# Performance work log

Hardware: AMD Instinct MI355X
Metric: run time of the kernel (lower is better)

The kernel has to match this reference:

```python
import jax, jax.numpy as jnp
import numpy as np

B, N, C = 128, 2048, 3
VL, PN = 256, 128  # vector_length, prediction_num
NEG_SLOPE = 0.01   # torch LeakyReLU default
BN_EPS = 1e-5


def _lin(key, fin, fout):
    k1, k2 = jax.random.split(key)
    lim = 1.0 / np.sqrt(fin)
    W = jax.random.uniform(k1, (fin, fout), minval=-lim, maxval=lim, dtype=jnp.float32)
    b = jax.random.uniform(k2, (fout,), minval=-lim, maxval=lim, dtype=jnp.float32)
    return W, b


def setup_inputs() -> dict:
    key = jax.random.key(0)
    ks = jax.random.split(key, 14)
    x = jax.random.normal(ks[0], (B, N, C), dtype=jnp.float32)
    lengths = jnp.maximum(jax.random.randint(ks[1], (B,), 0, N), 1).astype(jnp.int32)
    eps = jax.random.normal(ks[2], (B, VL), dtype=jnp.float32)
    W1, b1 = _lin(ks[3], C, 64)
    W2, b2 = _lin(ks[4], 64, 64)
    W3, b3 = _lin(ks[5], 64, 128)
    W4, b4 = _lin(ks[6], 128, 1024)
    Wf, bf = _lin(ks[7], 1024, 1024)
    Wmu, bmu = _lin(ks[8], 1024, VL)
    Wlv, blv = _lin(ks[9], 1024, VL)
    Wd1, bd1 = _lin(ks[10], VL, 1024)
    Wd2, bd2 = _lin(ks[11], 1024, 1024)
    Wd3, bd3 = _lin(ks[12], 1024, PN * C)
    g1 = jnp.ones((1024,), jnp.float32); be1 = jnp.zeros((1024,), jnp.float32)
    g2 = jnp.ones((1024,), jnp.float32); be2 = jnp.zeros((1024,), jnp.float32)
    return dict(x=x, lengths=lengths, eps=eps,
                W1=W1, b1=b1, W2=W2, b2=b2, W3=W3, b3=b3, W4=W4, b4=b4,
                Wf=Wf, bf=bf, Wmu=Wmu, bmu=bmu, Wlv=Wlv, blv=blv,
                Wd1=Wd1, bd1=bd1, g1=g1, be1=be1,
                Wd2=Wd2, bd2=bd2, g2=g2, be2=be2,
                Wd3=Wd3, bd3=bd3)


def _lrelu(h):
    return jnp.where(h > 0, h, NEG_SLOPE * h)


def _bn(h, g, b):
    # BatchNorm1d in training mode: biased batch stats
    m = h.mean(axis=0)
    v = h.var(axis=0)
    return (h - m) * jax.lax.rsqrt(v + BN_EPS) * g + b


def reference(x, lengths, eps,
              W1, b1, W2, b2, W3, b3, W4, b4,
              Wf, bf, Wmu, bmu, Wlv, blv,
              Wd1, bd1, g1, be1, Wd2, bd2, g2, be2, Wd3, bd3):
    # --- pointnet per-point MLP (batched over padded [B,N,C]) ---
    h = _lrelu(x @ W1 + b1)          # [B,N,64]
    h = _lrelu(h @ W2 + b2)          # [B,N,64]
    h = _lrelu(h @ W3 + b3)          # [B,N,128]
    h = _lrelu(h @ W4 + b4)          # [B,N,1024]
    # masked max over points (ragged -> padded+mask)
    mask = jnp.arange(N)[None, :] < lengths[:, None]   # [B,N]
    h = jnp.where(mask[:, :, None], h, -jnp.inf)
    pooled = jnp.max(h, axis=1)      # [B,1024]
    # --- encoder head ---
    e = _lrelu(pooled @ Wf + bf)
    mu = e @ Wmu + bmu               # [B,VL]
    logvar = e @ Wlv + blv           # [B,VL]
    # --- reparameterize ---
    z = mu + eps * jnp.exp(0.5 * logvar)
    # --- decoder: Linear+BN+LeakyReLU x2, final Linear ---
    d = _lrelu(_bn(z @ Wd1 + bd1, g1, be1))
    d = _lrelu(_bn(d @ Wd2 + bd2, g2, be2))
    y = (d @ Wd3 + bd3).reshape(-1, PN, C)   # [B,PN,C]
    return (y, mu, logvar)
```

## Files before the change

### kernel.cpp

```cpp
#include <hip/hip_runtime.h>
#include <hip/hip_bf16.h>
#include <math.h>

#define NEG_SLOPE 0.01f

typedef short short8 __attribute__((ext_vector_type(8)));
typedef float f32x4 __attribute__((ext_vector_type(4)));

__device__ __forceinline__ float lrelu(float v) { return v > 0.0f ? v : NEG_SLOPE * v; }

__device__ __forceinline__ short f2bf(float f) {
    __hip_bfloat16 h = __float2bfloat16(f);
    return __builtin_bit_cast(short, h);
}

__global__ __launch_bounds__(256) void pack_all(
    const float* __restrict__ W4, const float* __restrict__ Wf,
    const float* __restrict__ Wmu, const float* __restrict__ Wlv,
    const float* __restrict__ Wd1, const float* __restrict__ Wd2,
    const float* __restrict__ Wd3, const float* __restrict__ W2,
    const float* __restrict__ W3,
    short* __restrict__ F4, short* __restrict__ Ff, short* __restrict__ Fmuvl,
    short* __restrict__ Fd1, short* __restrict__ Fd2, short* __restrict__ Fd3,
    short* __restrict__ F2, short* __restrict__ F3)
{
    int bid = blockIdx.x;
    const float* src = nullptr; short* dst = nullptr; int K = 0, N = 0; int muvl = 0;
    if      (bid < 64)   { src = W4;  dst = F4;    K = 128;  N = 1024; }
    else if (bid < 576)  { src = Wf;  dst = Ff;    K = 1024; N = 1024; bid -= 64; }
    else if (bid < 832)  { src = nullptr; dst = Fmuvl; K = 1024; N = 512; muvl = 1; bid -= 576; }
    else if (bid < 960)  { src = Wd1; dst = Fd1;   K = 256;  N = 1024; bid -= 832; }
    else if (bid < 1472) { src = Wd2; dst = Fd2;   K = 1024; N = 1024; bid -= 960; }
    else if (bid < 1664) { src = Wd3; dst = Fd3;   K = 1024; N = 384;  bid -= 1472; }
    else if (bid < 1666) { src = W2;  dst = F2;    K = 64;   N = 64;   bid -= 1664; }
    else                 { src = W3;  dst = F3;    K = 64;   N = 128;  bid -= 1666; }

    const int fragid = bid * 4 + (threadIdx.x >> 6);
    const int lane   = threadIdx.x & 63;
    const int K32    = K >> 5;
    const int t   = fragid / (K32 * 4);
    const int rem = fragid - t * K32 * 4;
    const int ks  = rem >> 2;
    const int n   = rem & 3;
    const int col   = t * 64 + n * 16 + (lane & 15);
    const int kbase = ks * 32 + (lane >> 4) * 8;

    short8 v;
#pragma unroll
    for (int e = 0; e < 8; ++e) {
        float f;
        if (muvl) f = (col < 256) ? Wmu[(size_t)(kbase + e) * 256 + col]
                                  : Wlv[(size_t)(kbase + e) * 256 + col - 256];
        else      f = src[(size_t)(kbase + e) * N + col];
        v[e] = f2bf(f);
    }
    *(short8*)&dst[(size_t)fragid * 512 + lane * 8] = v;
}

__global__ __launch_bounds__(128, 2) void h3_kernel(
    const float* __restrict__ x, const int* __restrict__ lengths,
    const float* __restrict__ W1, const float* __restrict__ b1,
    const float* __restrict__ b2, const float* __restrict__ b3,
    const short* __restrict__ F2, const short* __restrict__ F3,
    short* __restrict__ h3p)
{
    const int tid  = threadIdx.x;
    const int b    = blockIdx.x & 127;
    const int c2   = blockIdx.x >> 7;
    const int lane = tid & 63;
    const int w    = tid >> 6;
    const int g    = c2 * 2 + w;
    const int len  = lengths[b];
    if (g * 64 >= len) return;

    __shared__ short S[16384];
    short* Aw = S + w * 8192;
    const int gid = b * 2048 + g * 64 + lane;

    {
        const float x0 = x[gid * 3 + 0];
        const float x1 = x[gid * 3 + 1];
        const float x2 = x[gid * 3 + 2];
#pragma unroll
        for (int q = 0; q < 8; ++q) {
            short8 pv;
#pragma unroll
            for (int e = 0; e < 8; ++e) {
                int c = q * 8 + e;
                float v = b1[c];
                v = fmaf(x0, W1[c], v);
                v = fmaf(x1, W1[64 + c], v);
                v = fmaf(x2, W1[128 + c], v);
                pv[e] = f2bf(lrelu(v));
            }
            *(short8*)&Aw[lane * 64 + ((q ^ (lane & 7)) * 8)] = pv;
        }
    }

    {
        short8 a2[4][2];
#pragma unroll
        for (int m = 0; m < 4; ++m)
#pragma unroll
            for (int ks = 0; ks < 2; ++ks) {
                int rl = m * 16 + (lane & 15);
                int kch = ks * 4 + (lane >> 4);
                a2[m][ks] = *(const short8*)&Aw[rl * 64 + ((kch ^ (rl & 7)) * 8)];
            }
        short8 b2f[2][4];
#pragma unroll
        for (int ks = 0; ks < 2; ++ks)
#pragma unroll
            for (int n = 0; n < 4; ++n)
                b2f[ks][n] = *(const short8*)&F2[(size_t)(ks * 4 + n) * 512 + lane * 8];

        f32x4 acc2[4][4];
#pragma unroll
        for (int m = 0; m < 4; ++m)
#pragma unroll
            for (int n = 0; n < 4; ++n) acc2[m][n] = 0;
#pragma unroll
        for (int ks = 0; ks < 2; ++ks)
#pragma unroll
            for (int n = 0; n < 4; ++n)
#pragma unroll
                for (int m = 0; m < 4; ++m)
                    acc2[m][n] = __builtin_amdgcn_mfma_f32_16x16x32_bf16(
                        a2[m][ks], b2f[ks][n], acc2[m][n], 0, 0, 0);

#pragma unroll
        for (int n = 0; n < 4; ++n) {
            int col = n * 16 + (lane & 15);
            float bv = b2[col];
            int colch = col >> 3;
#pragma unroll
            for (int m = 0; m < 4; ++m)
#pragma unroll
                for (int r = 0; r < 4; ++r) {
                    int rl = m * 16 + (lane >> 4) * 4 + r;
                    Aw[4096 + rl * 64 + ((colch ^ (rl & 7)) * 8) + (col & 7)] =
                        f2bf(lrelu(acc2[m][n][r] + bv));
                }
        }
    }

    {
        short8 a3[4][2];
#pragma unroll
        for (int m = 0; m < 4; ++m)
#pragma unroll
            for (int ks = 0; ks < 2; ++ks) {
                int rl = m * 16 + (lane & 15);
                int kch = ks * 4 + (lane >> 4);
                a3[m][ks] = *(const short8*)&Aw[4096 + rl * 64 + ((kch ^ (rl & 7)) * 8)];
            }
#pragma unroll
        for (int half = 0; half < 2; ++half) {
            short8 b3f[2][4];
#pragma unroll
            for (int ks = 0; ks < 2; ++ks)
#pragma unroll
                for (int n = 0; n < 4; ++n)
                    b3f[ks][n] = *(const short8*)&F3[(size_t)(half * 8 + ks * 4 + n) * 512 + lane * 8];

            f32x4 acc3[4][4];
#pragma unroll
            for (int m = 0; m < 4; ++m)
#pragma unroll
                for (int n = 0; n < 4; ++n) acc3[m][n] = 0;
#pragma unroll
            for (int ks = 0; ks < 2; ++ks)
#pragma unroll
                for (int n = 0; n < 4; ++n)
#pragma unroll
                    for (int m = 0; m < 4; ++m)
                        acc3[m][n] = __builtin_amdgcn_mfma_f32_16x16x32_bf16(
                            a3[m][ks], b3f[ks][n], acc3[m][n], 0, 0, 0);

#pragma unroll
            for (int n = 0; n < 4; ++n) {
                int col = half * 64 + n * 16 + (lane & 15);
                float bv = b3[col];
                int colch = col >> 3;
#pragma unroll
                for (int m = 0; m < 4; ++m)
#pragma unroll
                    for (int r = 0; r < 4; ++r) {
                        int rl = m * 16 + (lane >> 4) * 4 + r;
                        Aw[rl * 128 + ((colch ^ (rl & 7)) * 8) + (col & 7)] =
                            f2bf(lrelu(acc3[m][n][r] + bv));
                    }
            }
        }
    }

    const size_t obase = ((size_t)(b * 32 + g) * 16) * 512 + lane * 8;
#pragma unroll
    for (int ks = 0; ks < 4; ++ks)
#pragma unroll
        for (int m = 0; m < 4; ++m) {
            int rl = m * 16 + (lane & 15);
            int ch = (ks * 4 + (lane >> 4)) ^ (rl & 7);
            short8 af = *(const short8*)&Aw[rl * 128 + ch * 8];
            *(short8*)&h3p[obase + (size_t)(ks * 4 + m) * 512] = af;
        }
}

__global__ __launch_bounds__(256, 3) void l4_pool_kernel(
    const short* __restrict__ h3p, const int* __restrict__ lengths,
    const short* __restrict__ F4, float* __restrict__ part)
{
    const int tid = threadIdx.x, lane = tid & 63, w = tid >> 6;
    const int b = blockIdx.x, ch = blockIdx.y, rh = blockIdx.z;
    const int len = lengths[b];
    const int live32 = (len + 31) >> 5;
    const int cbeg = rh * 32;
    int cend = (rh + 1) * 32; if (cend > live32) cend = live32;
    if (cbeg >= cend) return;

    __shared__ short L[8192];

    const int t = ch * 4 + w;
    short8 bfr[4][4];
#pragma unroll
    for (int ks = 0; ks < 4; ++ks)
#pragma unroll
        for (int n = 0; n < 4; ++n)
            bfr[ks][n] = *(const short8*)&F4[(size_t)((t * 4 + ks) * 4 + n) * 512 + lane * 8];

    const int cfull = len >> 5;
    float madd[2][4];
#pragma unroll
    for (int m = 0; m < 2; ++m)
#pragma unroll
        for (int rr = 0; rr < 4; ++rr)
            madd[m][rr] = (m * 16 + (lane >> 4) * 4 + rr < (len & 31)) ? 0.0f : -INFINITY;

    f32x4 rmax[4];
#pragma unroll
    for (int n = 0; n < 4; ++n)
#pragma unroll
        for (int rr = 0; rr < 4; ++rr) rmax[n][rr] = -INFINITY;

    const size_t bb = (size_t)b * 32;
    short8 stg[2];
    {
        int c64 = cbeg >> 1, mh = cbeg & 1;
#pragma unroll
        for (int pass = 0; pass < 2; ++pass) {
            int idx = pass * 256 + tid, fi = idx >> 6, li = idx & 63;
            stg[pass] = *(const short8*)&h3p[((bb + c64) * 16 + (fi >> 1) * 4 + mh * 2 + (fi & 1)) * 512 + li * 8];
        }
#pragma unroll
        for (int pass = 0; pass < 2; ++pass)
            *(short8*)&L[(pass * 256 + tid) * 8] = stg[pass];
    }
    __syncthreads();

    for (int c = cbeg; c < cend; ++c) {
        const int p = (c - cbeg) & 1;
        if (c + 1 < cend) {
            int c64 = (c + 1) >> 1, mh = (c + 1) & 1;
#pragma unroll
            for (int pass = 0; pass < 2; ++pass) {
                int idx = pass * 256 + tid, fi = idx >> 6, li = idx & 63;
                stg[pass] = *(const short8*)&h3p[((bb + c64) * 16 + (fi >> 1) * 4 + mh * 2 + (fi & 1)) * 512 + li * 8];
            }
        }

        const short* Lb = L + p * 4096;
        f32x4 acc[2][4];
#pragma unroll
        for (int m = 0; m < 2; ++m)
#pragma unroll
            for (int n = 0; n < 4; ++n) acc[m][n] = 0;
#pragma unroll
        for (int ks = 0; ks < 4; ++ks) {
            short8 a0 = *(const short8*)&Lb[(ks * 2 + 0) * 512 + lane * 8];
            short8 a1 = *(const short8*)&Lb[(ks * 2 + 1) * 512 + lane * 8];
#pragma unroll
            for (int n = 0; n < 4; ++n) {
                acc[0][n] = __builtin_amdgcn_mfma_f32_16x16x32_bf16(a0, bfr[ks][n], acc[0][n], 0, 0, 0);
                acc[1][n] = __builtin_amdgcn_mfma_f32_16x16x32_bf16(a1, bfr[ks][n], acc[1][n], 0, 0, 0);
            }
        }
        if (c < cfull) {
#pragma unroll
            for (int n = 0; n < 4; ++n)
#pragma unroll
                for (int rr = 0; rr < 4; ++rr)
                    rmax[n][rr] = fmaxf(rmax[n][rr], fmaxf(acc[0][n][rr], acc[1][n][rr]));
        } else {
#pragma unroll
            for (int n = 0; n < 4; ++n)
#pragma unroll
                for (int rr = 0; rr < 4; ++rr)
                    rmax[n][rr] = fmaxf(rmax[n][rr],
                        fmaxf(acc[0][n][rr] + madd[0][rr], acc[1][n][rr] + madd[1][rr]));
        }
        __syncthreads();
        if (c + 1 < cend) {
            short* Ln = L + (p ^ 1) * 4096;
#pragma unroll
            for (int pass = 0; pass < 2; ++pass)
                *(short8*)&Ln[(pass * 256 + tid) * 8] = stg[pass];
            __syncthreads();
        }
    }

#pragma unroll
    for (int n = 0; n < 4; ++n) {
        float v = fmaxf(fmaxf(rmax[n][0], rmax[n][1]), fmaxf(rmax[n][2], rmax[n][3]));
        v = fmaxf(v, __shfl_xor(v, 16));
        v = fmaxf(v, __shfl_xor(v, 32));
        if (lane < 16)
            part[((size_t)b * 2 + rh) * 1024 + ch * 256 + w * 64 + n * 16 + lane] = v;
    }
}

__global__ __launch_bounds__(256) void reduce_pool_kernel(
    const float* __restrict__ part, const int* __restrict__ lengths,
    const float* __restrict__ b4, short* __restrict__ pooled)
{
    const int b = blockIdx.x;
    const bool two = lengths[b] > 1024;
    for (int i = threadIdx.x; i < 1024; i += 256) {
        float m = part[((size_t)b * 2 + 0) * 1024 + i];
        if (two) m = fmaxf(m, part[((size_t)b * 2 + 1) * 1024 + i]);
        pooled[(size_t)b * 1024 + i] = f2bf(lrelu(m + b4[i]));
    }
}

template<int K32, int EPI>
__global__ __launch_bounds__(64) void gemm16(
    const short* __restrict__ A, const short* __restrict__ Wfrag,
    const float* __restrict__ bias, const float* __restrict__ bias2,
    float* __restrict__ outF, float* __restrict__ outF2,
    short* __restrict__ outB, int Nout)
{
    const int lane = threadIdx.x;
    const int cbb = blockIdx.x, rh = blockIdx.y;
    const int K = K32 * 32;
    const int t = cbb >> 2, n = cbb & 3;

    short8 bf[K32];
#pragma unroll
    for (int ks = 0; ks < K32; ++ks)
        bf[ks] = *(const short8*)&Wfrag[(size_t)((t * K32 + ks) * 4 + n) * 512 + lane * 8];

    const int arow0 = rh * 32 + (lane & 15);
    const int koff  = (lane >> 4) * 8;
    f32x4 acc[2];
    acc[0] = 0; acc[1] = 0;
#pragma unroll
    for (int ks = 0; ks < K32; ++ks) {
        short8 a0 = *(const short8*)&A[(size_t)arow0 * K + ks * 32 + koff];
        short8 a1 = *(const short8*)&A[(size_t)(arow0 + 16) * K + ks * 32 + koff];
        acc[0] = __builtin_amdgcn_mfma_f32_16x16x32_bf16(a0, bf[ks], acc[0], 0, 0, 0);
        acc[1] = __builtin_amdgcn_mfma_f32_16x16x32_bf16(a1, bf[ks], acc[1], 0, 0, 0);
    }

    const int c0 = cbb * 16;
    const int cl = lane & 15;
    if (EPI == 2) {
        const float* bs = (c0 < 256) ? bias : bias2;
        float* of = (c0 < 256) ? outF : outF2;
        int col = (c0 & 255) + cl;
        float bv = bs[col];
#pragma unroll
        for (int m = 0; m < 2; ++m)
#pragma unroll
            for (int rr = 0; rr < 4; ++rr) {
                int row = rh * 32 + m * 16 + (lane >> 4) * 4 + rr;
                of[(size_t)row * 256 + col] = acc[m][rr] + bv;
            }
    } else {
        int col = c0 + cl;
        float bv = bias[col];
#pragma unroll
        for (int m = 0; m < 2; ++m)
#pragma unroll
            for (int rr = 0; rr < 4; ++rr) {
                int row = rh * 32 + m * 16 + (lane >> 4) * 4 + rr;
                float v = acc[m][rr] + bv;
                if (EPI == 1) outB[(size_t)row * Nout + col] = f2bf(lrelu(v));
                else          outF[(size_t)row * Nout + col] = v;
            }
    }
}

template<int K32, bool ZIN>
__global__ __launch_bounds__(256) void gemmBN(
    const short* __restrict__ A, const float* __restrict__ muv,
    const float* __restrict__ lvv, const float* __restrict__ eps,
    const short* __restrict__ Wfrag,
    const float* __restrict__ g, const float* __restrict__ be,
    short* __restrict__ outB, int Nout)
{
    __shared__ float bns[4][16];
    __shared__ float bnq[4][16];

    const int tid = threadIdx.x, lane = tid & 63, w = tid >> 6;
    const int cbb = blockIdx.x;
    const int K = K32 * 32;
    const int t = cbb >> 2, n = cbb & 3;

    short8 bf[K32];
#pragma unroll
    for (int ks = 0; ks < K32; ++ks)
        bf[ks] = *(const short8*)&Wfrag[(size_t)((t * K32 + ks) * 4 + n) * 512 + lane * 8];

    const int arow0 = w * 32 + (lane & 15);
    const int koff  = (lane >> 4) * 8;
    f32x4 acc[2];
    acc[0] = 0; acc[1] = 0;
#pragma unroll
    for (int ks = 0; ks < K32; ++ks) {
        short8 a0, a1;
        if (ZIN) {
#pragma unroll
            for (int e = 0; e < 8; ++e) {
                int k = ks * 32 + koff + e;
                size_t i0 = (size_t)arow0 * 256 + k;
                size_t i1 = (size_t)(arow0 + 16) * 256 + k;
                a0[e] = f2bf(fmaf(eps[i0], expf(0.5f * lvv[i0]), muv[i0]));
                a1[e] = f2bf(fmaf(eps[i1], expf(0.5f * lvv[i1]), muv[i1]));
            }
        } else {
            a0 = *(const short8*)&A[(size_t)arow0 * K + ks * 32 + koff];
            a1 = *(const short8*)&A[(size_t)(arow0 + 16) * K + ks * 32 + koff];
        }
        acc[0] = __builtin_amdgcn_mfma_f32_16x16x32_bf16(a0, bf[ks], acc[0], 0, 0, 0);
        acc[1] = __builtin_amdgcn_mfma_f32_16x16x32_bf16(a1, bf[ks], acc[1], 0, 0, 0);
    }

    float s = 0.f, q = 0.f;
#pragma unroll
    for (int m = 0; m < 2; ++m)
#pragma unroll
        for (int rr = 0; rr < 4; ++rr) {
            float v = acc[m][rr];
            s += v; q = fmaf(v, v, q);
        }
    s += __shfl_xor(s, 16); s += __shfl_xor(s, 32);
    q += __shfl_xor(q, 16); q += __shfl_xor(q, 32);
    if (lane < 16) { bns[w][lane] = s; bnq[w][lane] = q; }
    __syncthreads();

    const int cl = lane & 15;
    float st = bns[0][cl] + bns[1][cl] + bns[2][cl] + bns[3][cl];
    float qt = bnq[0][cl] + bnq[1][cl] + bnq[2][cl] + bnq[3][cl];
    float mean = st * (1.0f / 128.0f);
    float var  = qt * (1.0f / 128.0f) - mean * mean;
    float rs   = 1.0f / sqrtf(var + 1e-5f);
    const int col = cbb * 16 + cl;
    float gg = g[col] * rs;
    float bb = be[col] - mean * gg;

#pragma unroll
    for (int m = 0; m < 2; ++m)
#pragma unroll
        for (int rr = 0; rr < 4; ++rr) {
            int row = w * 32 + m * 16 + (lane >> 4) * 4 + rr;
            outB[(size_t)row * Nout + col] = f2bf(lrelu(fmaf(acc[m][rr], gg, bb)));
        }
}

extern "C" void kernel_launch(void* const* d_in, const int* in_sizes, int n_in,
                              void* d_out, int out_size, void* d_ws, size_t ws_size,
                              hipStream_t stream)
{
    const float* x       = (const float*)d_in[0];
    const int*   lengths = (const int*)  d_in[1];
    const float* eps     = (const float*)d_in[2];
    const float* W1  = (const float*)d_in[3];  const float* b1  = (const float*)d_in[4];
    const float* W2  = (const float*)d_in[5];  const float* b2  = (const float*)d_in[6];
    const float* W3  = (const float*)d_in[7];  const float* b3  = (const float*)d_in[8];
    const float* W4  = (const float*)d_in[9];  const float* b4  = (const float*)d_in[10];
    const float* Wf  = (const float*)d_in[11]; const float* bf  = (const float*)d_in[12];
    const float* Wmu = (const float*)d_in[13]; const float* bmu = (const float*)d_in[14];
    const float* Wlv = (const float*)d_in[15]; const float* blv = (const float*)d_in[16];
    const float* Wd1 = (const float*)d_in[17];
    const float* g1  = (const float*)d_in[19]; const float* be1 = (const float*)d_in[20];
    const float* Wd2 = (const float*)d_in[21];
    const float* g2  = (const float*)d_in[23]; const float* be2 = (const float*)d_in[24];
    const float* Wd3 = (const float*)d_in[25]; const float* bd3 = (const float*)d_in[26];

    float* out = (float*)d_out;
    float* y_out  = out;
    float* mu_out = out + 49152;
    float* lv_out = out + 81920;

    char* ws = (char*)d_ws;
    short* F4    = (short*)(ws + 0);
    short* Ff    = (short*)(ws + 262144);
    short* Fmuvl = (short*)(ws + 2359296);
    short* Fd1   = (short*)(ws + 3407872);
    short* Fd2   = (short*)(ws + 3932160);
    short* Fd3   = (short*)(ws + 6029312);
    short* F2    = (short*)(ws + 6815744);
    short* F3    = (short*)(ws + 6823936);
    short* h3p   = (short*)(ws + 6840320);
    float* part  = (float*)(ws + 73949184);
    short* pooled = (short*)(ws + 74997760);
    short* ebuf   = (short*)(ws + 75259904);
    short* d1v    = (short*)(ws + 75522048);
    short* d2v    = (short*)(ws + 75784192);

    pack_all<<<1670, 256, 0, stream>>>(W4, Wf, Wmu, Wlv, Wd1, Wd2, Wd3, W2, W3,
                                       F4, Ff, Fmuvl, Fd1, Fd2, Fd3, F2, F3);
    h3_kernel<<<2048, 128, 0, stream>>>(x, lengths, W1, b1, b2, b3, F2, F3, h3p);
    l4_pool_kernel<<<dim3(128, 4, 2), 256, 0, stream>>>(h3p, lengths, F4, part);
    reduce_pool_kernel<<<128, 256, 0, stream>>>(part, lengths, b4, pooled);
    gemm16<32, 1><<<dim3(64, 4), 64, 0, stream>>>(pooled, Ff, bf, nullptr,
                                                  nullptr, nullptr, ebuf, 1024);
    gemm16<32, 2><<<dim3(32, 4), 64, 0, stream>>>(ebuf, Fmuvl, bmu, blv,
                                                  mu_out, lv_out, nullptr, 256);
    gemmBN<8, true><<<64, 256, 0, stream>>>(nullptr, mu_out, lv_out, eps,
                                            Fd1, g1, be1, d1v, 1024);
    gemmBN<32, false><<<64, 256, 0, stream>>>(d1v, nullptr, nullptr, nullptr,
                                              Fd2, g2, be2, d2v, 1024);
    gemm16<32, 0><<<dim3(24, 4), 64, 0, stream>>>(d2v, Fd3, bd3, nullptr,
                                                  y_out, nullptr, nullptr, 384);
}
```

Baseline: 122.6 us.

## Drop LDS staging in layer-4 pool; per-wave 128-col tiles with register double-buffering

The layer-4 GEMM+maxpool kernel no longer stages activations through shared memory with barriers. Each wave now loads its 16-row A fragments straight from global into registers, double-buffered, and covers 128 output columns, so the B fragments held in registers double. Work is split into 16-row chunks over 4 row-quarters instead of 32-row chunks over 2 halves, which trims masked waste on ragged lengths, and the reduce kernel combines up to 4 partials. Smaller buffers are moved into the no-longer-needed h3p region. The cost is more registers, with occupancy lowered to 2 blocks, and each wave reads A from global/L2 itself.

```diff
diff --git a/kernel.cpp b/kernel.cpp
--- a/kernel.cpp
+++ b/kernel.cpp
@@ -206,115 +206,91 @@
         }
 }
 
-__global__ __launch_bounds__(256, 3) void l4_pool_kernel(
+#define L4_LD(BUF, C)                                                         \
+    do {                                                                      \
+        const int g_ = (C) >> 2, m_ = (C) & 3;                                \
+        const size_t fb_ = ((size_t)(b * 32 + g_) * 16 + m_) * 512 + lane * 8;\
+        _Pragma("unroll")                                                     \
+        for (int ks = 0; ks < 4; ++ks)                                        \
+            BUF[ks] = *(const short8*)&h3p[fb_ + (size_t)(ks * 4) * 512];     \
+    } while (0)
+
+#define L4_FOLD(BUF, C)                                                       \
+    do {                                                                      \
+        f32x4 acc[8];                                                         \
+        _Pragma("unroll")                                                     \
+        for (int n = 0; n < 8; ++n) acc[n] = 0;                               \
+        _Pragma("unroll")                                                     \
+        for (int ks = 0; ks < 4; ++ks)                                        \
+            _Pragma("unroll")                                                 \
+            for (int n = 0; n < 8; ++n)                                       \
+                acc[n] = __builtin_amdgcn_mfma_f32_16x16x32_bf16(             \
+                    BUF[ks], bfr[ks][n], acc[n], 0, 0, 0);                    \
+        if ((C) == partial) {                                                 \
+            _Pragma("unroll")                                                 \
+            for (int n = 0; n < 8; ++n)                                       \
+                _Pragma("unroll")                                             \
+                for (int rr = 0; rr < 4; ++rr)                                \
+                    rmax[n][rr] = fmaxf(rmax[n][rr], acc[n][rr] + madd[rr]);  \
+        } else {                                                              \
+            _Pragma("unroll")                                                 \
+            for (int n = 0; n < 8; ++n)                                       \
+                _Pragma("unroll")                                             \
+                for (int rr = 0; rr < 4; ++rr)                                \
+                    rmax[n][rr] = fmaxf(rmax[n][rr], acc[n][rr]);             \
+        }                                                                     \
+    } while (0)
+
+__global__ __launch_bounds__(256, 2) void l4_pool_kernel(
     const short* __restrict__ h3p, const int* __restrict__ lengths,
     const short* __restrict__ F4, float* __restrict__ part)
 {
     const int tid = threadIdx.x, lane = tid & 63, w = tid >> 6;
-    const int b = blockIdx.x, ch = blockIdx.y, rh = blockIdx.z;
+    const int b = blockIdx.x, cgh = blockIdx.y, rq = blockIdx.z;
+    const int cg = cgh * 4 + w;
     const int len = lengths[b];
-    const int live32 = (len + 31) >> 5;
-    const int cbeg = rh * 32;
-    int cend = (rh + 1) * 32; if (cend > live32) cend = live32;
+    const int CH16 = (len + 15) >> 4;
+    const int cbeg = rq * 32;
+    int cend = cbeg + 32; if (cend > CH16) cend = CH16;
     if (cbeg >= cend) return;
 
-    __shared__ short L[8192];
-
-    const int t = ch * 4 + w;
-    short8 bfr[4][4];
+    short8 bfr[4][8];
 #pragma unroll
     for (int ks = 0; ks < 4; ++ks)
 #pragma unroll
-        for (int n = 0; n < 4; ++n)
-            bfr[ks][n] = *(const short8*)&F4[(size_t)((t * 4 + ks) * 4 + n) * 512 + lane * 8];
-
-    const int cfull = len >> 5;
-    float madd[2][4];
-#pragma unroll
-    for (int m = 0; m < 2; ++m)
-#pragma unroll
-        for (int rr = 0; rr < 4; ++rr)
-            madd[m][rr] = (m * 16 + (lane >> 4) * 4 + rr < (len & 31)) ? 0.0f : -INFINITY;
-
-    f32x4 rmax[4];
-#pragma unroll
-    for (int n = 0; n < 4; ++n)
+        for (int n = 0; n < 8; ++n)
+            bfr[ks][n] = *(const short8*)&F4[
+                (size_t)(((cg * 2 + (n >> 2)) * 4 + ks) * 4 + (n & 3)) * 512 + lane * 8];
+
+    const int partial = (len & 15) ? (CH16 - 1) : -1;
+    float madd[4];
+#pragma unroll
+    for (int rr = 0; rr < 4; ++rr)
+        madd[rr] = ((CH16 - 1) * 16 + (lane >> 4) * 4 + rr < len) ? 0.0f : -INFINITY;
+
+    f32x4 rmax[8];
+#pragma unroll
+    for (int n = 0; n < 8; ++n)
 #pragma unroll
         for (int rr = 0; rr < 4; ++rr) rmax[n][rr] = -INFINITY;
 
-    const size_t bb = (size_t)b * 32;
-    short8 stg[2];
-    {
-        int c64 = cbeg >> 1, mh = cbeg & 1;
-#pragma unroll
-        for (int pass = 0; pass < 2; ++pass) {
-            int idx = pass * 256 + tid, fi = idx >> 6, li = idx & 63;
-            stg[pass] = *(const short8*)&h3p[((bb + c64) * 16 + (fi >> 1) * 4 + mh * 2 + (fi & 1)) * 512 + li * 8];
-        }
-#pragma unroll
-        for (int pass = 0; pass < 2; ++pass)
-            *(short8*)&L[(pass * 256 + tid) * 8] = stg[pass];
-    }
-    __syncthreads();
-
-    for (int c = cbeg; c < cend; ++c) {
-        const int p = (c - cbeg) & 1;
-        if (c + 1 < cend) {
-            int c64 = (c + 1) >> 1, mh = (c + 1) & 1;
-#pragma unroll
-            for (int pass = 0; pass < 2; ++pass) {
-                int idx = pass * 256 + tid, fi = idx >> 6, li = idx & 63;
-                stg[pass] = *(const short8*)&h3p[((bb + c64) * 16 + (fi >> 1) * 4 + mh * 2 + (fi & 1)) * 512 + li * 8];
-            }
-        }
-
-        const short* Lb = L + p * 4096;
-        f32x4 acc[2][4];
-#pragma unroll
-        for (int m = 0; m < 2; ++m)
-#pragma unroll
-            for (int n = 0; n < 4; ++n) acc[m][n] = 0;
-#pragma unroll
-        for (int ks = 0; ks < 4; ++ks) {
-            short8 a0 = *(const short8*)&Lb[(ks * 2 + 0) * 512 + lane * 8];
-            short8 a1 = *(const short8*)&Lb[(ks * 2 + 1) * 512 + lane * 8];
-#pragma unroll
-            for (int n = 0; n < 4; ++n) {
-                acc[0][n] = __builtin_amdgcn_mfma_f32_16x16x32_bf16(a0, bfr[ks][n], acc[0][n], 0, 0, 0);
-                acc[1][n] = __builtin_amdgcn_mfma_f32_16x16x32_bf16(a1, bfr[ks][n], acc[1][n], 0, 0, 0);
-            }
-        }
-        if (c < cfull) {
-#pragma unroll
-            for (int n = 0; n < 4; ++n)
-#pragma unroll
-                for (int rr = 0; rr < 4; ++rr)
-                    rmax[n][rr] = fmaxf(rmax[n][rr], fmaxf(acc[0][n][rr], acc[1][n][rr]));
-        } else {
-#pragma unroll
-            for (int n = 0; n < 4; ++n)
-#pragma unroll
-                for (int rr = 0; rr < 4; ++rr)
-                    rmax[n][rr] = fmaxf(rmax[n][rr],
-                        fmaxf(acc[0][n][rr] + madd[0][rr], acc[1][n][rr] + madd[1][rr]));
-        }
-        __syncthreads();
-        if (c + 1 < cend) {
-            short* Ln = L + (p ^ 1) * 4096;
-#pragma unroll
-            for (int pass = 0; pass < 2; ++pass)
-                *(short8*)&Ln[(pass * 256 + tid) * 8] = stg[pass];
-            __syncthreads();
-        }
-    }
-
-#pragma unroll
-    for (int n = 0; n < 4; ++n) {
-        float v = fmaxf(fmaxf(rmax[n][0], rmax[n][1]), fmaxf(rmax[n][2], rmax[n][3]));
+    short8 aA[4], aB[4];
+    L4_LD(aA, cbeg);
+    for (int c = cbeg; c < cend; c += 2) {
+        if (c + 1 < cend) L4_LD(aB, c + 1);
+        L4_FOLD(aA, c);
+        if (c + 2 < cend) L4_LD(aA, c + 2);
+        if (c + 1 < cend) L4_FOLD(aB, c + 1);
+    }
+
+#pragma unroll
+    for (int n = 0; n < 8; ++n) {
+        float v = fmaxf(fmaxf(rmax[n][0], rmax[n][1]),
+                        fmaxf(rmax[n][2], rmax[n][3]));
         v = fmaxf(v, __shfl_xor(v, 16));
         v = fmaxf(v, __shfl_xor(v, 32));
         if (lane < 16)
-            part[((size_t)b * 2 + rh) * 1024 + ch * 256 + w * 64 + n * 16 + lane] = v;
+            part[((size_t)b * 4 + rq) * 1024 + cg * 128 + n * 16 + lane] = v;
     }
 }
 
@@ -323,10 +299,11 @@
     const float* __restrict__ b4, short* __restrict__ pooled)
 {
     const int b = blockIdx.x;
-    const bool two = lengths[b] > 1024;
+    int nlive = (lengths[b] + 511) >> 9;
     for (int i = threadIdx.x; i < 1024; i += 256) {
-        float m = part[((size_t)b * 2 + 0) * 1024 + i];
-        if (two) m = fmaxf(m, part[((size_t)b * 2 + 1) * 1024 + i]);
+        float m = part[((size_t)b * 4 + 0) * 1024 + i];
+        for (int j = 1; j < nlive; ++j)
+            m = fmaxf(m, part[((size_t)b * 4 + j) * 1024 + i]);
         pooled[(size_t)b * 1024 + i] = f2bf(lrelu(m + b4[i]));
     }
 }
@@ -502,15 +479,15 @@
     short* F3    = (short*)(ws + 6823936);
     short* h3p   = (short*)(ws + 6840320);
     float* part  = (float*)(ws + 73949184);
-    short* pooled = (short*)(ws + 74997760);
-    short* ebuf   = (short*)(ws + 75259904);
-    short* d1v    = (short*)(ws + 75522048);
-    short* d2v    = (short*)(ws + 75784192);
+    short* pooled = (short*)(ws + 6840320 + 0);
+    short* ebuf   = (short*)(ws + 6840320 + 262144);
+    short* d1v    = (short*)(ws + 6840320 + 524288);
+    short* d2v    = (short*)(ws + 6840320 + 786432);
 
     pack_all<<<1670, 256, 0, stream>>>(W4, Wf, Wmu, Wlv, Wd1, Wd2, Wd3, W2, W3,
                                        F4, Ff, Fmuvl, Fd1, Fd2, Fd3, F2, F3);
     h3_kernel<<<2048, 128, 0, stream>>>(x, lengths, W1, b1, b2, b3, F2, F3, h3p);
-    l4_pool_kernel<<<dim3(128, 4, 2), 256, 0, stream>>>(h3p, lengths, F4, part);
+    l4_pool_kernel<<<dim3(128, 2, 4), 256, 0, stream>>>(h3p, lengths, F4, part);
     reduce_pool_kernel<<<128, 256, 0, stream>>>(part, lengths, b4, pooled);
     gemm16<32, 1><<<dim3(64, 4), 64, 0, stream>>>(pooled, Ff, bf, nullptr,
                                                   nullptr, nullptr, ebuf, 1024);
```

New measurement: 144.2 us. +17.7%, slower.
